# Kernel tuning notes

Hardware: AMD Instinct MI355X
Metric: run time of the kernel (lower is better)

The kernel has to match this reference:

```python
import jax, jax.numpy as jnp
import numpy as np

T_MAX = 20  # max_seq_length


def setup_inputs() -> dict:
    key = jax.random.key(0)
    ks = jax.random.split(key, 24)
    B, H, A, V, Tc = 64, 512, 512, 50257, 19
    s = 0.02
    inp = {}
    inp["features"] = jax.random.normal(ks[0], (B, H), jnp.float32)
    inp["captions"] = jax.random.randint(ks[1], (B, Tc), 0, V)
    lens = jax.random.randint(ks[2], (B, 1), 1, T_MAX + 1)
    inp["lengths"] = -jnp.sort(-lens, axis=0)  # descending so sort_ind is identity
    inp["embed_table"] = jax.random.uniform(ks[3], (V, H), jnp.float32, -0.1, 0.1)
    # LSTM cell (PyTorch layout): input = [emb; attended] -> 2H
    inp["W_ih"] = jax.random.normal(ks[4], (4 * H, 2 * H), jnp.float32) * s
    inp["W_hh"] = jax.random.normal(ks[5], (4 * H, H), jnp.float32) * s
    inp["b_ih"] = jnp.zeros((4 * H,), jnp.float32)
    inp["b_hh"] = jnp.zeros((4 * H,), jnp.float32)
    # attention
    inp["W_enc"] = jax.random.normal(ks[6], (H, A), jnp.float32) * s
    inp["b_enc"] = jnp.zeros((A,), jnp.float32)
    inp["W_dec"] = jax.random.normal(ks[7], (H, A), jnp.float32) * s
    inp["b_dec"] = jnp.zeros((A,), jnp.float32)
    inp["W_full"] = jax.random.normal(ks[8], (A, 1), jnp.float32) * s
    inp["b_full"] = jnp.zeros((1,), jnp.float32)
    # init_h / init_c / f_beta / fc
    inp["W_hinit"] = jax.random.normal(ks[9], (H, H), jnp.float32) * s
    inp["b_hinit"] = jnp.zeros((H,), jnp.float32)
    inp["W_cinit"] = jax.random.normal(ks[10], (H, H), jnp.float32) * s
    inp["b_cinit"] = jnp.zeros((H,), jnp.float32)
    inp["W_beta"] = jax.random.normal(ks[11], (H, H), jnp.float32) * s
    inp["b_beta"] = jnp.zeros((H,), jnp.float32)
    inp["W_fc"] = jax.random.uniform(ks[12], (H, V), jnp.float32, -0.1, 0.1)
    inp["b_fc"] = jnp.zeros((V,), jnp.float32)
    return inp


def _decode(features, embed_table, W_ih, W_hh, b_ih, b_hh, W_enc, b_enc,
            W_dec, b_dec, W_full, b_full, W_hinit, b_hinit, W_cinit, b_cinit,
            W_beta, b_beta, W_fc, b_fc, captions, lengths):
    B, H = features.shape
    emb = embed_table[captions]                               # (B, T-1, H)
    embeddings = jnp.concatenate([features[:, None, :], emb], axis=1)  # (B, T, H)
    encoder_out = features[:, None, :]                        # (B, 1, H) num_pixels=1
    mean_enc = encoder_out.mean(axis=1)
    h0 = mean_enc @ W_hinit + b_hinit
    c0 = mean_enc @ W_cinit + b_cinit
    att1 = encoder_out @ W_enc + b_enc                        # (B, 1, A), time-invariant
    lens = lengths[:, 0]

    def step(carry, xs):
        h, c = carry
        emb_t, t = xs
        # attention
        att2 = h @ W_dec + b_dec                              # (B, A)
        e = jax.nn.relu(att1 + att2[:, None, :]) @ W_full + b_full  # (B, 1, 1)
        alpha = jax.nn.softmax(e[..., 0], axis=1)             # (B, 1)
        awe = (encoder_out * alpha[..., None]).sum(axis=1)    # (B, H)
        gate = jax.nn.sigmoid(h @ W_beta + b_beta)
        awe = gate * awe
        # LSTM cell (PyTorch gate order i, f, g, o)
        x = jnp.concatenate([emb_t, awe], axis=1)             # (B, 2H)
        gates = x @ W_ih.T + b_ih + h @ W_hh.T + b_hh
        i, f, g, o = jnp.split(gates, 4, axis=1)
        c_new = jax.nn.sigmoid(f) * c + jax.nn.sigmoid(i) * jnp.tanh(g)
        h_new = jax.nn.sigmoid(o) * jnp.tanh(c_new)
        preds = h_new @ W_fc + b_fc                           # (B, V)
        mask = (t < lens)[:, None]
        h = jnp.where(mask, h_new, h)
        c = jnp.where(mask, c_new, c)
        out_t = jnp.where(mask, preds, jnp.zeros_like(preds))
        return (h, c), out_t

    xs = (embeddings.transpose(1, 0, 2), jnp.arange(T_MAX))
    _, outs = jax.lax.scan(step, (h0, c0), xs)                # (T, B, V)
    return outs.transpose(1, 0, 2)                            # (B, T, V)


def reference(features, captions, lengths, embed_table, W_ih, W_hh, b_ih, b_hh,
              W_enc, b_enc, W_dec, b_dec, W_full, b_full, W_hinit, b_hinit,
              W_cinit, b_cinit, W_beta, b_beta, W_fc, b_fc):
    return _decode(features, embed_table, W_ih, W_hh, b_ih, b_hh, W_enc, b_enc,
                   W_dec, b_dec, W_full, b_full, W_hinit, b_hinit, W_cinit,
                   b_cinit, W_beta, b_beta, W_fc, b_fc, captions, lengths)
```

## Files before the change

kernel.cpp:

```cpp
#include <hip/hip_runtime.h>
#include <hip/hip_bf16.h>


#define VV 50257
#define VP 50304
#define TT 20
#define NWRK 32
#define NTILES 6288
#define NNT 393

typedef __attribute__((ext_vector_type(4))) float f32x4;
typedef __attribute__((ext_vector_type(8))) short bf16x8;

#define MFMA(a,b,c) __builtin_amdgcn_mfma_f32_16x16x32_bf16((a),(b),(c),0,0,0)

__device__ __forceinline__ unsigned short f2bf(float f){
  union { float f; unsigned int u; } v; v.f = f;
  unsigned int u = v.u;
  return (unsigned short)((u + 0x7FFFu + ((u >> 16) & 1u)) >> 16);
}
__device__ __forceinline__ float sigf(float x){ return 1.f/(1.f + expf(-x)); }

__device__ __forceinline__ void gload_lds16(const unsigned short* g, unsigned short* l){
  __builtin_amdgcn_global_load_lds(
      (const __attribute__((address_space(1))) unsigned int*)g,
      (__attribute__((address_space(3))) unsigned int*)l, 16, 0, 0);
}

__device__ __forceinline__ void co_load16(bf16x8* d, const unsigned short* p){
  asm volatile("global_load_dwordx4 %0, %1, off sc0 sc1" : "=v"(*d) : "v"(p));
}
__device__ __forceinline__ void co_store2(unsigned short* p, unsigned short v){
  asm volatile("global_store_short %0, %1, off sc0 sc1" :: "v"(p), "v"(v) : "memory");
}
__device__ __forceinline__ unsigned int co_load_u32(const unsigned int* p){
  unsigned int r;
  asm volatile("global_load_dword %0, %1, off sc0 sc1\n\ts_waitcnt vmcnt(0)"
               : "=v"(r) : "v"(p) : "memory");
  return r;
}
__device__ __forceinline__ void co_store_u32(unsigned int* p, unsigned int v){
  asm volatile("global_store_dword %0, %1, off sc0 sc1" :: "v"(p), "v"(v) : "memory");
}

__device__ __forceinline__ void gbar(unsigned int* wflags, unsigned int* pflags,
                                     int widx, unsigned target){
  asm volatile("s_waitcnt vmcnt(0)" ::: "memory");
  __syncthreads();
  if(threadIdx.x == 0){
    co_store_u32(pflags + widx, target);
    co_store_u32(wflags + widx, target);
  }
  if(threadIdx.x < 64){
    const unsigned int* p = wflags + (threadIdx.x & 31);
    for(;;){
      unsigned v = co_load_u32(p);
      if(__all((int)(v >= target))) break;
      __builtin_amdgcn_s_sleep(1);
    }
  }
  __syncthreads();
}

__global__ __launch_bounds__(256) void prep(const float* __restrict__ Wih,
    const float* __restrict__ Whh, unsigned short* __restrict__ Wcomb,
    unsigned short* __restrict__ We,
    const float* __restrict__ Wbeta, unsigned short* __restrict__ Wbt,
    const float* __restrict__ feat, const float* __restrict__ emb,
    const int* __restrict__ cap, unsigned short* __restrict__ EmbMat,
    const float* __restrict__ Whi, const float* __restrict__ bhi,
    const float* __restrict__ Wci, const float* __restrict__ bci,
    unsigned short* __restrict__ xbuf, float* __restrict__ cbuf){
  __shared__ float tile[64][65];
  const int blk = blockIdx.x, tid = threadIdx.x;
  if(blk < 2048){
    int j = blk;
    for(int q=0;q<4;q++){ int k = tid + 256*q;
      float v = (k < 512) ? Whh[j*512 + k] : Wih[j*1024 + k];
      Wcomb[(size_t)j*1024 + k] = f2bf(v); }
    for(int q=0;q<2;q++){ int k = tid + 256*q;
      We[(size_t)j*512 + k] = f2bf(Wih[j*1024 + k]); }
  } else if(blk < 2112){
    int tb = blk - 2048;
    int c0 = (tb & 7)*64, r0 = (tb >> 3)*64;
    int tx = tid & 63, ty = tid >> 6;
    for(int i=0;i<16;i++){
      int r = ty + i*4;
      tile[r][tx] = Wbeta[(size_t)(r0+r)*512 + c0 + tx];
    }
    __syncthreads();
    for(int i=0;i<16;i++){
      int cl = ty + i*4;
      Wbt[(size_t)(c0+cl)*512 + r0 + tx] = f2bf(tile[tx][cl]);
    }
  } else if(blk < 3392){
    int m = blk - 2112; int t = m >> 6, b = m & 63;
    const float* src = (t == 0) ? (feat + b*512) : (emb + (size_t)cap[b*19 + (t-1)]*512);
    for(int q=0;q<2;q++){ int k = tid + 256*q;
      EmbMat[(size_t)m*512 + k] = f2bf(src[k]); }
  } else {
    int b = blk - 3392;
    float ah0 = bhi[tid], ah1 = bhi[tid+256];
    float ac0 = bci[tid], ac1 = bci[tid+256];
    for(int k=0;k<512;k++){
      float f = feat[b*512 + k];
      ah0 += f * Whi[k*512 + tid];     ah1 += f * Whi[k*512 + tid + 256];
      ac0 += f * Wci[k*512 + tid];     ac1 += f * Wci[k*512 + tid + 256];
    }
    xbuf[b*512 + tid] = f2bf(ah0);  xbuf[b*512 + tid + 256] = f2bf(ah1);
    cbuf[b*512 + tid] = ac0;        cbuf[b*512 + tid + 256] = ac1;
  }
}

__global__ __launch_bounds__(256) void gemmE(const unsigned short* __restrict__ Abf,
    const unsigned short* __restrict__ Bbf, const float* __restrict__ bias1,
    const float* __restrict__ bias2, float* __restrict__ Cout, int MT){
  __shared__ __align__(16) unsigned short As[128*64];
  __shared__ __align__(16) unsigned short Bs[128*64];
  const int nwg = gridDim.x;
  const int id = blockIdx.x;
  const int q = nwg >> 3, rr = nwg & 7;
  const int xcd = id & 7, pos = id >> 3;
  const int work = (xcd < rr) ? (xcd*(q+1) + pos) : (rr*(q+1) + (xcd-rr)*q + pos);
  const int m0 = (work % MT) * 128;
  const int n0 = (work / MT) * 128;
  const int tid = threadIdx.x, lane = tid & 63, w = tid >> 6;
  const int wr = w >> 1, wc = w & 1;
  const int lrow = lane >> 3, lcol = (lane & 7) * 8;
  const int l15 = lane & 15, lhi = lane >> 4;

  f32x4 acc[4][4];
#pragma unroll
  for(int i=0;i<4;i++)
#pragma unroll
    for(int j=0;j<4;j++) acc[i][j] = f32x4{0.f,0.f,0.f,0.f};

  for(int k0=0;k0<512;k0+=64){
    __syncthreads();
#pragma unroll
    for(int i=0;i<4;i++){
      int c = w*4 + i;
      int row = c*8 + lrow;
      gload_lds16(Abf + (size_t)(m0+row)*512 + k0 + lcol, As + c*512);
      gload_lds16(Bbf + (size_t)(n0+row)*512 + k0 + lcol, Bs + c*512);
    }
    asm volatile("s_waitcnt vmcnt(0)" ::: "memory");
    __syncthreads();
#pragma unroll
    for(int kk=0;kk<64;kk+=32){
      bf16x8 af[4], bfv[4];
#pragma unroll
      for(int mf=0;mf<4;mf++)
        af[mf] = *(const bf16x8*)(As + (wr*64 + mf*16 + l15)*64 + kk + lhi*8);
#pragma unroll
      for(int nf=0;nf<4;nf++)
        bfv[nf] = *(const bf16x8*)(Bs + (wc*64 + nf*16 + l15)*64 + kk + lhi*8);
#pragma unroll
      for(int mf=0;mf<4;mf++)
#pragma unroll
        for(int nf=0;nf<4;nf++)
          acc[mf][nf] = MFMA(af[mf], bfv[nf], acc[mf][nf]);
    }
  }
#pragma unroll
  for(int mf=0;mf<4;mf++)
#pragma unroll
    for(int nf=0;nf<4;nf++){
      int n = n0 + wc*64 + nf*16 + l15;
#pragma unroll
      for(int r=0;r<4;r++){
        int m = m0 + wr*64 + mf*16 + lhi*4 + r;
        int gate = n >> 9, col = n & 511;
        Cout[((size_t)m*512 + col)*4 + gate] = acc[mf][nf][r] + bias1[n] + bias2[n];
      }
    }
}

__global__ __launch_bounds__(256) void recur(
    const unsigned short* __restrict__ Wcomb,
    const unsigned short* __restrict__ Wbt,
    const float* __restrict__ bbeta,
    const float* __restrict__ feat,
    const float* __restrict__ E4,
    const float* __restrict__ c0,
    const int* __restrict__ lens,
    unsigned short* xbuf,
    unsigned short* awbuf,
    unsigned short* hs,
    unsigned int* ctrs,
    const float* __restrict__ Wfc, unsigned short* Wfct,
    const float* __restrict__ bfc, float* __restrict__ out){
  extern __shared__ char LDS[];
  int* lsh = (int*)LDS;
  const int tid = threadIdx.x;

  if(tid == 0){
    unsigned xcc = 99;
    asm volatile("s_getreg_b32 %0, hwreg(HW_REG_XCC_ID)" : "=s"(xcc));
    unsigned my = 0xffffffffu;
    if(xcc == 0) my = atomicAdd(&ctrs[0], 1u);
    lsh[0] = (my < NWRK) ? 1 : 0;
    lsh[1] = (int)my;
  }
  __syncthreads();
  const int iswork = lsh[0];
  const int widx = lsh[1];
  unsigned int* wflags = &ctrs[32];
  unsigned int* pflags = &ctrs[64];
  __syncthreads();

  if(!iswork){
    const int lane = tid & 63, w = tid >> 6;
    const int l15 = lane & 15, lhi = lane >> 4;
    unsigned short* Bs = (unsigned short*)LDS;
    float* et = (float*)(LDS + 131072);
    float (*tile)[65] = (float(*)[65])LDS;
    int* tk = (int*)(LDS + 147456);
    bool tdone = false;

    int lnv[4];
#pragma unroll
    for(int r=0;r<4;r++) lnv[r] = lens[w*16 + lhi*4 + r];

    for(;;){
      __syncthreads();
      if(tid == 0) *tk = (int)atomicAdd(&ctrs[1], 1u);
      __syncthreads();
      int j = *tk;
      __syncthreads();
      if(j >= NTILES + NNT) return;

      if(j < NTILES){
        int c0t = (j % 786)*64, r0 = (j / 786)*64;
        int tx = tid & 63, ty = tid >> 6;
        for(int i=0;i<16;i++){
          int r = ty + i*4; int sc = c0t + tx;
          tile[r][tx] = (sc < VV) ? Wfc[(size_t)(r0+r)*VV + sc] : 0.f;
        }
        __syncthreads();
        for(int i=0;i<16;i++){
          int cl = ty + i*4;
          co_store2(Wfct + (size_t)(c0t+cl)*512 + r0 + tx, f2bf(tile[tx][cl]));
        }
        asm volatile("s_waitcnt vmcnt(0)" ::: "memory");
        __syncthreads();
        if(tid == 0) atomicAdd(&ctrs[2], 1u);
        continue;
      }

      if(!tdone){
        if(tid == 0){
          while(co_load_u32(&ctrs[2]) < NTILES) __builtin_amdgcn_s_sleep(16);
        }
        __syncthreads();
        tdone = true;
      }
      const int nt = j - NTILES;
      const int n0 = nt * 128;
#pragma unroll
      for(int i=0;i<32;i++){
        int cid = tid + 256*i;
        int row = cid >> 6, cc = cid & 63;
        bf16x8 v = *(const bf16x8*)(Wfct + (size_t)(n0 + row)*512 + cc*8);
        *(bf16x8*)((char*)Bs + row*1024 + ((cc*16) ^ ((row & 7) << 4))) = v;
      }
      float bias[8];
#pragma unroll
      for(int nf=0;nf<8;nf++){
        int n = n0 + nf*16 + l15;
        bias[nf] = (n < VV) ? bfc[n] : 0.f;
      }
      __syncthreads();
      const bool edge = (n0 + 128 > VV);

      for(int t=0;t<TT;t++){
        if(tid < 64){
          const unsigned int* p = pflags + (tid & 31);
          unsigned tgt = (unsigned)(2*t + 2);
          for(;;){
            unsigned v = co_load_u32(p);
            if(__all((int)(v >= tgt))) break;
            __builtin_amdgcn_s_sleep(8);
          }
        }
        __syncthreads();
        bf16x8 af[16];
        const unsigned short* pA = hs + (size_t)(t*64 + w*16 + l15)*512 + lhi*8;
#pragma unroll
        for(int i=0;i<16;i++) co_load16(&af[i], pA + i*32);
        asm volatile("s_waitcnt vmcnt(0)" ::: "memory");
        __builtin_amdgcn_sched_barrier(0);
        f32x4 acc[8];
#pragma unroll
        for(int nf=0;nf<8;nf++) acc[nf] = f32x4{0.f,0.f,0.f,0.f};
#pragma unroll
        for(int i=0;i<16;i++){
          int kb2 = i*64 + lhi*16;
#pragma unroll
          for(int nf=0;nf<8;nf++){
            int gr = nf*16 + l15;
            bf16x8 bv = *(const bf16x8*)((char*)Bs + gr*1024 + (kb2 ^ ((gr & 7) << 4)));
            acc[nf] = MFMA(af[i], bv, acc[nf]);
          }
        }
        for(int h=0; h<2; h++){
          __syncthreads();
          if((w >> 1) == h){
#pragma unroll
            for(int nf=0;nf<8;nf++){
#pragma unroll
              for(int r=0;r<4;r++){
                bool valid = t < lnv[r];
                float v = valid ? (acc[nf][r] + bias[nf]) : 0.f;
                et[((w & 1)*16 + lhi*4 + r)*128 + nf*16 + l15] = v;
              }
            }
          }
          __syncthreads();
#pragma unroll
          for(int qq=0;qq<4;qq++){
            int idx = tid + 256*qq;
            int rowl = idx >> 5, c4 = idx & 31;
            int b = h*32 + rowl;
            const float* er = et + rowl*128;
            size_t bdw = (size_t)(b*20 + t)*VV + n0;
            if(!edge){
              int al = (int)((4 - (bdw & 3)) & 3);
              int chunks = (128 - al) >> 2;
              int tail = (128 - al) & 3;
              if(c4 < chunks){
                int s0 = al + c4*4;
                f32x4 v; v[0]=er[s0]; v[1]=er[s0+1]; v[2]=er[s0+2]; v[3]=er[s0+3];
                *(f32x4*)(out + bdw + s0) = v;
              }
              if(c4 < al) out[bdw + c4] = er[c4];
              if(c4 < tail){ int s1 = al + chunks*4 + c4; out[bdw + s1] = er[s1]; }
            } else {
#pragma unroll
              for(int i2=0;i2<4;i2++){
                int cg = n0 + c4*4 + i2;
                if(cg < VV) out[bdw + (c4*4 + i2)] = er[c4*4 + i2];
              }
            }
          }
        }
      }
    }
  }

  char* WCb = LDS;
  char* WBb = LDS + 131072;
  const int lane = tid & 63, w = tid >> 6;
  const int l15 = lane & 15, lhi = lane >> 4;
  const int jj0 = widx * 16;
  const int jj = jj0 + l15;
  const int arow = w*16 + l15;

  for(int cid = tid; cid < 8192; cid += 256){
    int gr = cid >> 7, cc = cid & 127;
    size_t gg = (size_t)(gr >> 4)*512 + jj0 + (gr & 15);
    bf16x8 v = *(const bf16x8*)(Wcomb + gg*1024 + cc*8);
    *(bf16x8*)(WCb + gr*2048 + ((cc*16) ^ ((gr & 7) << 4))) = v;
  }
  for(int cid = tid; cid < 1024; cid += 256){
    int r = cid >> 6, cc = cid & 63;
    bf16x8 v = *(const bf16x8*)(Wbt + (size_t)(jj0 + r)*512 + cc*8);
    *(bf16x8*)(WBb + r*1024 + ((cc*16) ^ ((r & 7) << 4))) = v;
  }

  float c_reg[4], fe[4]; int ln[4]; unsigned short hold[4];
#pragma unroll
  for(int r=0;r<4;r++){
    int b = w*16 + lhi*4 + r;
    c_reg[r] = c0[b*512 + jj];
    fe[r]    = feat[b*512 + jj];
    ln[r]    = lens[b];
    hold[r]  = xbuf[b*512 + jj];
  }
  const float bb = bbeta[jj];
  const unsigned short* pAx = xbuf  + (size_t)arow*512 + lhi*8;
  const unsigned short* pAw = awbuf + (size_t)arow*512 + lhi*8;
  __syncthreads();

  for(int t=0;t<TT;t++){
    f32x4 e4v[4];
#pragma unroll
    for(int r=0;r<4;r++){
      int b = w*16 + lhi*4 + r;
      e4v[r] = *(const f32x4*)(E4 + (((size_t)(t*64 + b))*512 + jj)*4);
    }
    bf16x8 a[16];
#pragma unroll
    for(int i=0;i<16;i++) co_load16(&a[i], pAx + i*32);
    asm volatile("s_waitcnt vmcnt(0)" ::: "memory");
    __builtin_amdgcn_sched_barrier(0);

    f32x4 acca = f32x4{0.f,0.f,0.f,0.f};
    f32x4 accg[4];
#pragma unroll
    for(int i=0;i<4;i++) accg[i] = f32x4{0.f,0.f,0.f,0.f};
#pragma unroll
    for(int i=0;i<16;i++){
      int kb2 = i*64 + lhi*16;
      bf16x8 wb = *(const bf16x8*)(WBb + l15*1024 + (kb2 ^ ((l15 & 7) << 4)));
      acca = MFMA(a[i], wb, acca);
#pragma unroll
      for(int nf=0; nf<4; nf++){
        int gr = nf*16 + l15;
        bf16x8 wg = *(const bf16x8*)(WCb + gr*2048 + (kb2 ^ ((gr & 7) << 4)));
        accg[nf] = MFMA(a[i], wg, accg[nf]);
      }
    }
#pragma unroll
    for(int r=0;r<4;r++){
      int b = w*16 + lhi*4 + r;
      float g = sigf(acca[r] + bb);
      co_store2(awbuf + b*512 + jj, f2bf(g * fe[r]));
    }
    gbar(wflags, pflags, widx, (unsigned)(2*t+1));

#pragma unroll
    for(int i=0;i<16;i++) co_load16(&a[i], pAw + i*32);
    asm volatile("s_waitcnt vmcnt(0)" ::: "memory");
    __builtin_amdgcn_sched_barrier(0);
#pragma unroll
    for(int i=0;i<16;i++){
      int kb2 = 1024 + i*64 + lhi*16;
#pragma unroll
      for(int nf=0; nf<4; nf++){
        int gr = nf*16 + l15;
        bf16x8 wg = *(const bf16x8*)(WCb + gr*2048 + (kb2 ^ ((gr & 7) << 4)));
        accg[nf] = MFMA(a[i], wg, accg[nf]);
      }
    }

#pragma unroll
    for(int r=0;r<4;r++){
      int b = w*16 + lhi*4 + r;
      float iv = sigf(accg[0][r] + e4v[r][0]);
      float fv = sigf(accg[1][r] + e4v[r][1]);
      float gv = tanhf(accg[2][r] + e4v[r][2]);
      float ov = sigf(accg[3][r] + e4v[r][3]);
      float cn = fv*c_reg[r] + iv*gv;
      float hn = ov * tanhf(cn);
      bool valid = t < ln[r];
      if(valid) c_reg[r] = cn;
      unsigned short hb = valid ? f2bf(hn) : hold[r];
      hold[r] = hb;
      co_store2(hs + (size_t)(t*64 + b)*512 + jj, hb);
      co_store2(xbuf + b*512 + jj, hb);
    }
    gbar(wflags, pflags, widx, (unsigned)(2*t+2));
  }
}

extern "C" void kernel_launch(void* const* d_in, const int* in_sizes, int n_in,
                              void* d_out, int out_size, void* d_ws, size_t ws_size,
                              hipStream_t stream){
  const float* feat  = (const float*)d_in[0];
  const int*   cap   = (const int*)  d_in[1];
  const int*   lens  = (const int*)  d_in[2];
  const float* emb   = (const float*)d_in[3];
  const float* Wih   = (const float*)d_in[4];
  const float* Whh   = (const float*)d_in[5];
  const float* bih   = (const float*)d_in[6];
  const float* bhh   = (const float*)d_in[7];
  const float* Whi   = (const float*)d_in[14];
  const float* bhi   = (const float*)d_in[15];
  const float* Wci   = (const float*)d_in[16];
  const float* bci   = (const float*)d_in[17];
  const float* Wbeta = (const float*)d_in[18];
  const float* bbeta = (const float*)d_in[19];
  const float* Wfc   = (const float*)d_in[20];
  const float* bfc   = (const float*)d_in[21];
  float* out = (float*)d_out;

  char* ws = (char*)d_ws;
  size_t off = 0;
  auto alloc = [&](size_t bytes)->void*{
    void* p = ws + off; off += (bytes + 1023) & ~(size_t)1023; return p; };
  unsigned short* Wcomb  = (unsigned short*)alloc((size_t)2048*1024*2);
  unsigned short* We     = (unsigned short*)alloc((size_t)2048*512*2);
  unsigned short* Wbt    = (unsigned short*)alloc((size_t)512*512*2);
  unsigned short* Wfct   = (unsigned short*)alloc((size_t)VP*512*2);
  unsigned short* EmbMat = (unsigned short*)alloc((size_t)1280*512*2);
  float*          E4     = (float*)alloc((size_t)1280*2048*4);
  unsigned short* xbuf   = (unsigned short*)alloc((size_t)64*512*2);
  unsigned short* awbuf  = (unsigned short*)alloc((size_t)64*512*2);
  float*          cbuf   = (float*)alloc((size_t)64*512*4);
  unsigned short* hs     = (unsigned short*)alloc((size_t)1280*512*2);
  unsigned int*   ctrs   = (unsigned int*)alloc(512);

  static_cast<void>(hipFuncSetAttribute((const void*)recur,
      hipFuncAttributeMaxDynamicSharedMemorySize, 148480));

  hipMemsetAsync(ctrs, 0, 512, stream);

  prep<<<3456, 256, 0, stream>>>(Wih, Whh, Wcomb, We, Wbeta, Wbt, feat, emb,
                                 cap, EmbMat, Whi, bhi, Wci, bci, xbuf, cbuf);

  gemmE<<<160, 256, 0, stream>>>(EmbMat, We, bih, bhh, E4, 10);

  recur<<<256, 256, 148480, stream>>>(Wcomb, Wbt, bbeta, feat, E4, cbuf, lens,
                                      xbuf, awbuf, hs, ctrs, Wfc, Wfct, bfc, out);
}
```

Before: 622.8 us.

## Move output projection GEMM out of persistent recurrence into separate kernel

The vocabulary projection, which had been overlapped per timestep inside the persistent recurrence kernel (non-worker blocks polled progress flags), is split into a standalone outgemm kernel launched after the recurrence finishes. The recurrence kernel now only runs the LSTM worker blocks plus W_fc transpose/convert helper blocks, launched with many more blocks to spread the transpose, and the barrier writes a single flag array. This removes cross-block polling and the coherent loads/stores, but gives up overlap between the recurrence and the large output GEMM, which now runs serially afterwards.

```diff
diff --git a/kernel.cpp b/kernel.cpp
--- a/kernel.cpp
+++ b/kernel.cpp
@@ -7,7 +7,6 @@
 #define TT 20
 #define NWRK 32
 #define NTILES 6288
-#define NNT 393
 
 typedef __attribute__((ext_vector_type(4))) float f32x4;
 typedef __attribute__((ext_vector_type(8))) short bf16x8;
@@ -43,16 +42,14 @@
   asm volatile("global_store_dword %0, %1, off sc0 sc1" :: "v"(p), "v"(v) : "memory");
 }
 
-__device__ __forceinline__ void gbar(unsigned int* wflags, unsigned int* pflags,
-                                     int widx, unsigned target){
+__device__ __forceinline__ void gbar(unsigned int* flags, int widx, unsigned target){
   asm volatile("s_waitcnt vmcnt(0)" ::: "memory");
   __syncthreads();
   if(threadIdx.x == 0){
-    co_store_u32(pflags + widx, target);
-    co_store_u32(wflags + widx, target);
+    co_store_u32(flags + widx, target);
   }
   if(threadIdx.x < 64){
-    const unsigned int* p = wflags + (threadIdx.x & 31);
+    const unsigned int* p = flags + (threadIdx.x & 31);
     for(;;){
       unsigned v = co_load_u32(p);
       if(__all((int)(v >= target))) break;
@@ -186,11 +183,12 @@
     const int* __restrict__ lens,
     unsigned short* xbuf,
     unsigned short* awbuf,
-    unsigned short* hs,
+    unsigned short* __restrict__ hs,
     unsigned int* ctrs,
-    const float* __restrict__ Wfc, unsigned short* Wfct,
-    const float* __restrict__ bfc, float* __restrict__ out){
+    const float* __restrict__ Wfc, unsigned short* __restrict__ Wfct){
   extern __shared__ char LDS[];
+  char* WCb = LDS;
+  char* WBb = LDS + 131072;
   int* lsh = (int*)LDS;
   const int tid = threadIdx.x;
 
@@ -205,161 +203,42 @@
   __syncthreads();
   const int iswork = lsh[0];
   const int widx = lsh[1];
-  unsigned int* wflags = &ctrs[32];
-  unsigned int* pflags = &ctrs[64];
   __syncthreads();
 
   if(!iswork){
-    const int lane = tid & 63, w = tid >> 6;
-    const int l15 = lane & 15, lhi = lane >> 4;
-    unsigned short* Bs = (unsigned short*)LDS;
-    float* et = (float*)(LDS + 131072);
     float (*tile)[65] = (float(*)[65])LDS;
-    int* tk = (int*)(LDS + 147456);
-    bool tdone = false;
-
-    int lnv[4];
-#pragma unroll
-    for(int r=0;r<4;r++) lnv[r] = lens[w*16 + lhi*4 + r];
-
+    int tx = tid & 63, ty = tid >> 6;
     for(;;){
       __syncthreads();
-      if(tid == 0) *tk = (int)atomicAdd(&ctrs[1], 1u);
-      __syncthreads();
-      int j = *tk;
-      __syncthreads();
-      if(j >= NTILES + NNT) return;
-
-      if(j < NTILES){
-        int c0t = (j % 786)*64, r0 = (j / 786)*64;
-        int tx = tid & 63, ty = tid >> 6;
-        for(int i=0;i<16;i++){
-          int r = ty + i*4; int sc = c0t + tx;
-          tile[r][tx] = (sc < VV) ? Wfc[(size_t)(r0+r)*VV + sc] : 0.f;
-        }
-        __syncthreads();
-        for(int i=0;i<16;i++){
-          int cl = ty + i*4;
-          co_store2(Wfct + (size_t)(c0t+cl)*512 + r0 + tx, f2bf(tile[tx][cl]));
-        }
-        asm volatile("s_waitcnt vmcnt(0)" ::: "memory");
-        __syncthreads();
-        if(tid == 0) atomicAdd(&ctrs[2], 1u);
-        continue;
-      }
-
-      if(!tdone){
-        if(tid == 0){
-          while(co_load_u32(&ctrs[2]) < NTILES) __builtin_amdgcn_s_sleep(16);
-        }
-        __syncthreads();
-        tdone = true;
-      }
-      const int nt = j - NTILES;
-      const int n0 = nt * 128;
-#pragma unroll
-      for(int i=0;i<32;i++){
-        int cid = tid + 256*i;
-        int row = cid >> 6, cc = cid & 63;
-        bf16x8 v = *(const bf16x8*)(Wfct + (size_t)(n0 + row)*512 + cc*8);
-        *(bf16x8*)((char*)Bs + row*1024 + ((cc*16) ^ ((row & 7) << 4))) = v;
-      }
-      float bias[8];
-#pragma unroll
-      for(int nf=0;nf<8;nf++){
-        int n = n0 + nf*16 + l15;
-        bias[nf] = (n < VV) ? bfc[n] : 0.f;
-      }
-      __syncthreads();
-      const bool edge = (n0 + 128 > VV);
-
-      for(int t=0;t<TT;t++){
-        if(tid < 64){
-          const unsigned int* p = pflags + (tid & 31);
-          unsigned tgt = (unsigned)(2*t + 2);
-          for(;;){
-            unsigned v = co_load_u32(p);
-            if(__all((int)(v >= tgt))) break;
-            __builtin_amdgcn_s_sleep(8);
-          }
-        }
-        __syncthreads();
-        bf16x8 af[16];
-        const unsigned short* pA = hs + (size_t)(t*64 + w*16 + l15)*512 + lhi*8;
-#pragma unroll
-        for(int i=0;i<16;i++) co_load16(&af[i], pA + i*32);
-        asm volatile("s_waitcnt vmcnt(0)" ::: "memory");
-        __builtin_amdgcn_sched_barrier(0);
-        f32x4 acc[8];
-#pragma unroll
-        for(int nf=0;nf<8;nf++) acc[nf] = f32x4{0.f,0.f,0.f,0.f};
-#pragma unroll
-        for(int i=0;i<16;i++){
-          int kb2 = i*64 + lhi*16;
-#pragma unroll
-          for(int nf=0;nf<8;nf++){
-            int gr = nf*16 + l15;
-            bf16x8 bv = *(const bf16x8*)((char*)Bs + gr*1024 + (kb2 ^ ((gr & 7) << 4)));
-            acc[nf] = MFMA(af[i], bv, acc[nf]);
-          }
-        }
-        for(int h=0; h<2; h++){
-          __syncthreads();
-          if((w >> 1) == h){
-#pragma unroll
-            for(int nf=0;nf<8;nf++){
-#pragma unroll
-              for(int r=0;r<4;r++){
-                bool valid = t < lnv[r];
-                float v = valid ? (acc[nf][r] + bias[nf]) : 0.f;
-                et[((w & 1)*16 + lhi*4 + r)*128 + nf*16 + l15] = v;
-              }
-            }
-          }
-          __syncthreads();
-#pragma unroll
-          for(int qq=0;qq<4;qq++){
-            int idx = tid + 256*qq;
-            int rowl = idx >> 5, c4 = idx & 31;
-            int b = h*32 + rowl;
-            const float* er = et + rowl*128;
-            size_t bdw = (size_t)(b*20 + t)*VV + n0;
-            if(!edge){
-              int al = (int)((4 - (bdw & 3)) & 3);
-              int chunks = (128 - al) >> 2;
-              int tail = (128 - al) & 3;
-              if(c4 < chunks){
-                int s0 = al + c4*4;
-                f32x4 v; v[0]=er[s0]; v[1]=er[s0+1]; v[2]=er[s0+2]; v[3]=er[s0+3];
-                *(f32x4*)(out + bdw + s0) = v;
-              }
-              if(c4 < al) out[bdw + c4] = er[c4];
-              if(c4 < tail){ int s1 = al + chunks*4 + c4; out[bdw + s1] = er[s1]; }
-            } else {
-#pragma unroll
-              for(int i2=0;i2<4;i2++){
-                int cg = n0 + c4*4 + i2;
-                if(cg < VV) out[bdw + (c4*4 + i2)] = er[c4*4 + i2];
-              }
-            }
-          }
-        }
-      }
-    }
-  }
-
-  char* WCb = LDS;
-  char* WBb = LDS + 131072;
+      if(tid == 0) lsh[0] = (int)atomicAdd(&ctrs[16], 1u);
+      __syncthreads();
+      int tb = lsh[0];
+      __syncthreads();
+      if(tb >= NTILES) return;
+      int c0t = (tb % 786)*64, r0 = (tb / 786)*64;
+      for(int i=0;i<16;i++){
+        int r = ty + i*4; int sc = c0t + tx;
+        tile[r][tx] = (sc < VV) ? Wfc[(size_t)(r0+r)*VV + sc] : 0.f;
+      }
+      __syncthreads();
+      for(int i=0;i<16;i++){
+        int cl = ty + i*4;
+        Wfct[(size_t)(c0t+cl)*512 + r0 + tx] = f2bf(tile[tx][cl]);
+      }
+    }
+  }
+
   const int lane = tid & 63, w = tid >> 6;
   const int l15 = lane & 15, lhi = lane >> 4;
   const int jj0 = widx * 16;
   const int jj = jj0 + l15;
   const int arow = w*16 + l15;
+  unsigned int* flags = &ctrs[32];
 
   for(int cid = tid; cid < 8192; cid += 256){
     int gr = cid >> 7, cc = cid & 127;
-    size_t gg = (size_t)(gr >> 4)*512 + jj0 + (gr & 15);
-    bf16x8 v = *(const bf16x8*)(Wcomb + gg*1024 + cc*8);
+    size_t g = (size_t)(gr >> 4)*512 + jj0 + (gr & 15);
+    bf16x8 v = *(const bf16x8*)(Wcomb + g*1024 + cc*8);
     *(bf16x8*)(WCb + gr*2048 + ((cc*16) ^ ((gr & 7) << 4))) = v;
   }
   for(int cid = tid; cid < 1024; cid += 256){
@@ -417,7 +296,7 @@
       float g = sigf(acca[r] + bb);
       co_store2(awbuf + b*512 + jj, f2bf(g * fe[r]));
     }
-    gbar(wflags, pflags, widx, (unsigned)(2*t+1));
+    gbar(flags, widx, (unsigned)(2*t+1));
 
 #pragma unroll
     for(int i=0;i<16;i++) co_load16(&a[i], pAw + i*32);
@@ -447,10 +326,102 @@
       if(valid) c_reg[r] = cn;
       unsigned short hb = valid ? f2bf(hn) : hold[r];
       hold[r] = hb;
-      co_store2(hs + (size_t)(t*64 + b)*512 + jj, hb);
+      hs[((size_t)(t*64 + b))*512 + jj] = hb;
       co_store2(xbuf + b*512 + jj, hb);
     }
-    gbar(wflags, pflags, widx, (unsigned)(2*t+2));
+    if(t < TT-1) gbar(flags, widx, (unsigned)(2*t+2));
+  }
+}
+
+__global__ __launch_bounds__(256) void outgemm(
+    const unsigned short* __restrict__ hs,
+    const unsigned short* __restrict__ Wfct,
+    const float* __restrict__ bfc, const int* __restrict__ lens,
+    float* __restrict__ out){
+  extern __shared__ char LDS[];
+  unsigned short* Bs = (unsigned short*)LDS;
+  float* et = (float*)(LDS + 131072);
+  const int tid = threadIdx.x, lane = tid & 63, w = tid >> 6;
+  const int l15 = lane & 15, lhi = lane >> 4;
+  const int n0 = blockIdx.x * 128;
+
+#pragma unroll
+  for(int i=0;i<32;i++){
+    int cid = tid + 256*i;
+    int row = cid >> 6, cc = cid & 63;
+    bf16x8 v = *(const bf16x8*)(Wfct + (size_t)(n0 + row)*512 + cc*8);
+    *(bf16x8*)((char*)Bs + row*1024 + ((cc*16) ^ ((row & 7) << 4))) = v;
+  }
+  float bias[8]; int lnv[4];
+#pragma unroll
+  for(int nf=0;nf<8;nf++){
+    int n = n0 + nf*16 + l15;
+    bias[nf] = (n < VV) ? bfc[n] : 0.f;
+  }
+#pragma unroll
+  for(int r=0;r<4;r++) lnv[r] = lens[w*16 + lhi*4 + r];
+  __syncthreads();
+  const bool edge = (n0 + 128 > VV);
+
+  for(int t=0;t<TT;t++){
+    bf16x8 af[16];
+    const unsigned short* pA = hs + (size_t)(t*64 + w*16 + l15)*512 + lhi*8;
+#pragma unroll
+    for(int i=0;i<16;i++) af[i] = *(const bf16x8*)(pA + i*32);
+    f32x4 acc[8];
+#pragma unroll
+    for(int nf=0;nf<8;nf++) acc[nf] = f32x4{0.f,0.f,0.f,0.f};
+#pragma unroll
+    for(int i=0;i<16;i++){
+      int kb2 = i*64 + lhi*16;
+#pragma unroll
+      for(int nf=0;nf<8;nf++){
+        int gr = nf*16 + l15;
+        bf16x8 bv = *(const bf16x8*)((char*)Bs + gr*1024 + (kb2 ^ ((gr & 7) << 4)));
+        acc[nf] = MFMA(af[i], bv, acc[nf]);
+      }
+    }
+    for(int h=0; h<2; h++){
+      __syncthreads();
+      if((w >> 1) == h){
+#pragma unroll
+        for(int nf=0;nf<8;nf++){
+#pragma unroll
+          for(int r=0;r<4;r++){
+            bool valid = t < lnv[r];
+            float v = valid ? (acc[nf][r] + bias[nf]) : 0.f;
+            et[((w & 1)*16 + lhi*4 + r)*128 + nf*16 + l15] = v;
+          }
+        }
+      }
+      __syncthreads();
+#pragma unroll
+      for(int qq=0;qq<4;qq++){
+        int idx = tid + 256*qq;
+        int rowl = idx >> 5, c4 = idx & 31;
+        int b = h*32 + rowl;
+        const float* er = et + rowl*128;
+        size_t bdw = (size_t)(b*20 + t)*VV + n0;
+        if(!edge){
+          int al = (int)((4 - (bdw & 3)) & 3);
+          int chunks = (128 - al) >> 2;
+          int tail = (128 - al) & 3;
+          if(c4 < chunks){
+            int s0 = al + c4*4;
+            f32x4 v; v[0]=er[s0]; v[1]=er[s0+1]; v[2]=er[s0+2]; v[3]=er[s0+3];
+            *(f32x4*)(out + bdw + s0) = v;
+          }
+          if(c4 < al) out[bdw + c4] = er[c4];
+          if(c4 < tail){ int s1 = al + chunks*4 + c4; out[bdw + s1] = er[s1]; }
+        } else {
+#pragma unroll
+          for(int i2=0;i2<4;i2++){
+            int cg = n0 + c4*4 + i2;
+            if(cg < VV) out[bdw + (c4*4 + i2)] = er[c4*4 + i2];
+          }
+        }
+      }
+    }
   }
 }
 
@@ -489,18 +460,22 @@
   unsigned short* awbuf  = (unsigned short*)alloc((size_t)64*512*2);
   float*          cbuf   = (float*)alloc((size_t)64*512*4);
   unsigned short* hs     = (unsigned short*)alloc((size_t)1280*512*2);
-  unsigned int*   ctrs   = (unsigned int*)alloc(512);
+  unsigned int*   ctrs   = (unsigned int*)alloc(256);
 
   static_cast<void>(hipFuncSetAttribute((const void*)recur,
-      hipFuncAttributeMaxDynamicSharedMemorySize, 148480));
-
-  hipMemsetAsync(ctrs, 0, 512, stream);
+      hipFuncAttributeMaxDynamicSharedMemorySize, 147456));
+  static_cast<void>(hipFuncSetAttribute((const void*)outgemm,
+      hipFuncAttributeMaxDynamicSharedMemorySize, 147456));
+
+  hipMemsetAsync(ctrs, 0, 256, stream);
 
   prep<<<3456, 256, 0, stream>>>(Wih, Whh, Wcomb, We, Wbeta, Wbt, feat, emb,
                                  cap, EmbMat, Whi, bhi, Wci, bci, xbuf, cbuf);
 
   gemmE<<<160, 256, 0, stream>>>(EmbMat, We, bih, bhh, E4, 10);
 
-  recur<<<256, 256, 148480, stream>>>(Wcomb, Wbt, bbeta, feat, E4, cbuf, lens,
-                                      xbuf, awbuf, hs, ctrs, Wfc, Wfct, bfc, out);
-}
+  recur<<<2080, 256, 147456, stream>>>(Wcomb, Wbt, bbeta, feat, E4, cbuf, lens,
+                                       xbuf, awbuf, hs, ctrs, Wfc, Wfct);
+
+  outgemm<<<393, 256, 147456, stream>>>(hs, Wfct, bfc, lens, out);
+}
```

After: 649.4 us. 1.04x slower.
